# Kernel tuning notes

Hardware: AMD Instinct MI355X
Metric: run time of the kernel (lower is better)

## Reference

```python
import jax, jax.numpy as jnp
import numpy as np

B, S, D, H = 2, 2048, 2048, 16
HD = D // H  # head_dim = 128
ROPE_BASE = 10000.0


def _rope_tables(seq_len, head_dim, base, dtype):
    inv_freq = 1.0 / (base ** (jnp.arange(0, head_dim, 2, dtype=jnp.float32) / head_dim))
    t = jnp.arange(seq_len, dtype=jnp.float32)
    freqs = jnp.einsum('s,d->sd', t, inv_freq)           # [S, HD/2]
    emb = jnp.concatenate([freqs, freqs], axis=-1)        # [S, HD]
    return jnp.cos(emb).astype(dtype), jnp.sin(emb).astype(dtype)


def _rotate_half(x):
    half = x.shape[-1] // 2
    return jnp.concatenate([-x[..., half:], x[..., :half]], axis=-1)


def setup_inputs() -> dict:
    key = jax.random.key(0)
    kx, kq, kk, kv, ko = jax.random.split(key, 5)
    std = 0.02
    return {
        'x': jax.random.normal(kx, (B, S, D), dtype=jnp.float32),
        'Wq': jax.random.normal(kq, (D, D), dtype=jnp.float32) * std,
        'Wk': jax.random.normal(kk, (D, D), dtype=jnp.float32) * std,
        'Wv': jax.random.normal(kv, (D, D), dtype=jnp.float32) * std,
        'Wo': jax.random.normal(ko, (D, D), dtype=jnp.float32) * std,
    }


def reference(x, Wq, Wk, Wv, Wo):
    b, s, d = x.shape
    scale = HD ** -0.5
    # projections (nn.Linear: x @ W.T), split heads -> [b, h, s, hd]
    q = (x @ Wq.T).reshape(b, s, H, HD).transpose(0, 2, 1, 3)
    k = (x @ Wk.T).reshape(b, s, H, HD).transpose(0, 2, 1, 3)
    v = (x @ Wv.T).reshape(b, s, H, HD).transpose(0, 2, 1, 3)
    cos, sin = _rope_tables(s, HD, ROPE_BASE, x.dtype)    # [s, hd]
    q = q * cos + _rotate_half(q) * sin
    k = k * cos + _rotate_half(k) * sin
    scores = jnp.einsum('bhqd,bhkd->bhqk', q, k) * scale  # [b,h,s,s]
    causal = jnp.triu(jnp.ones((s, s), dtype=bool), k=1)
    scores = jnp.where(causal, jnp.float32(-jnp.inf).astype(scores.dtype), scores)
    attn = jax.nn.softmax(scores, axis=-1)
    out = jnp.einsum('bhqk,bhkd->bhqd', attn, v)
    out = out.transpose(0, 2, 1, 3).reshape(b, s, d)
    return out @ Wo.T
```

## Files before the change

### kernel.cpp

```cpp
#include <hip/hip_runtime.h>
#include <hip/hip_bf16.h>
#include <cstdint>
#include <cstddef>

#define B_ 2
#define S_ 2048
#define D_ 2048
#define H_ 16
#define HD_ 128

typedef __bf16 bf16_t;
typedef __bf16 bf16x8 __attribute__((ext_vector_type(8)));
typedef __bf16 bf16x4 __attribute__((ext_vector_type(4)));
typedef short s16x4 __attribute__((ext_vector_type(4)));
typedef float f32x4 __attribute__((ext_vector_type(4)));

__device__ __forceinline__ void async16(const bf16_t* g, bf16_t* l) {
    __builtin_amdgcn_global_load_lds(
        (const __attribute__((address_space(1))) unsigned int*)g,
        (__attribute__((address_space(3))) unsigned int*)l, 16, 0, 0);
}

__device__ __forceinline__ f32x4 mfma16x16x16_bf16(bf16x4 a, bf16x4 b, f32x4 c) {
#if __has_builtin(__builtin_amdgcn_mfma_f32_16x16x16_bf16)
    return __builtin_amdgcn_mfma_f32_16x16x16_bf16(a, b, c, 0, 0, 0);
#elif __has_builtin(__builtin_amdgcn_mfma_f32_16x16x16bf16_1k)
    return __builtin_amdgcn_mfma_f32_16x16x16bf16_1k(
        __builtin_bit_cast(s16x4, a), __builtin_bit_cast(s16x4, b), c, 0, 0, 0);
#else
    f32x4 d = c;
    asm("v_mfma_f32_16x16x16_bf16 %0, %1, %2, %0" : "+v"(d) : "v"(a), "v"(b));
    return d;
#endif
}

__global__ void f2b_multi(const float* __restrict__ x, const float* __restrict__ wq,
                          const float* __restrict__ wk, const float* __restrict__ wv,
                          const float* __restrict__ wo, bf16_t* __restrict__ xb,
                          bf16_t* __restrict__ wqb, bf16_t* __restrict__ wkb,
                          bf16_t* __restrict__ wvb, bf16_t* __restrict__ wob) {
    const float* in; bf16_t* out;
    float sc = 1.0f;
    switch (blockIdx.y) {
        case 0: in = x;            out = xb;            break;
        case 1: in = x + 4194304;  out = xb + 4194304;  break;
        case 2: in = wq;           out = wqb; sc = 0.08838834764831845f; break;
        case 3: in = wk;           out = wkb;           break;
        case 4: in = wv;           out = wvb;           break;
        default: in = wo;          out = wob;           break;
    }
    int i = (blockIdx.x * blockDim.x + threadIdx.x) * 4;
    float4 v = *(const float4*)(in + i);
    bf16x4 o = { (bf16_t)(v.x * sc), (bf16_t)(v.y * sc), (bf16_t)(v.z * sc), (bf16_t)(v.w * sc) };
    *(bf16x4*)(out + i) = o;
}

__global__ void rope_kernel(bf16_t* __restrict__ q, bf16_t* __restrict__ k) {
    int idx = blockIdx.x * blockDim.x + threadIdx.x;
    bf16_t* p = (blockIdx.y == 0) ? q : k;
    int i0 = (idx & 7) * 8;
    int rest = idx >> 3;
    int h = rest & (H_ - 1);
    int row = rest >> 4;
    int s = row & (S_ - 1);
    size_t base = (size_t)row * D_ + (size_t)h * HD_ + i0;
    bf16x8 x0 = *(bf16x8*)(p + base);
    bf16x8 x1 = *(bf16x8*)(p + base + 64);
    bf16x8 o0, o1;
#pragma unroll
    for (int j = 0; j < 8; ++j) {
        float inv = __expf(-(float)(i0 + j) * 0.14391156831212787f);
        float ang = (float)s * inv;
        float sn, c;
        __sincosf(ang, &sn, &c);
        float a = (float)x0[j], bb = (float)x1[j];
        o0[j] = (bf16_t)(a * c - bb * sn);
        o1[j] = (bf16_t)(bb * c + a * sn);
    }
    *(bf16x8*)(p + base) = o0;
    *(bf16x8*)(p + base + 64) = o1;
}


__global__ __launch_bounds__(512, 2) void gemm_qkv(const bf16_t* __restrict__ A,
                                                   const bf16_t* __restrict__ Wq,
                                                   const bf16_t* __restrict__ Wk,
                                                   const bf16_t* __restrict__ Wv,
                                                   bf16_t* __restrict__ qb,
                                                   bf16_t* __restrict__ kb,
                                                   bf16_t* __restrict__ vtb) {
    __shared__ __align__(16) bf16_t lds[49152];
    const int K = D_;
    const int NT = K / 64;
    int t = threadIdx.x;
    int w = t >> 6, lane = t & 63, lo = lane & 15, hi = lane >> 4;
    int seg = blockIdx.x >> 4;
    int n0 = (blockIdx.x & 15) * 128;
    int m0 = blockIdx.y * 256;
    const bf16_t* Bt = (seg == 0) ? Wq : (seg == 1) ? Wk : Wv;
    int wm = w >> 2, wn = w & 3;
    f32x4 acc[8][2] = {};
    int srowA = w * 32 + (lane >> 3);
    int srowB = w * 16 + (lane >> 3);
    int scol = ((lane & 7) ^ (lane >> 3)) * 8;
    const bf16_t* gA = A  + (size_t)(m0 + srowA) * K + scol;
    const bf16_t* gB = Bt + (size_t)(n0 + srowB) * K + scol;

    auto STAGE = [&](int c, int kt) {
        bf16_t* dA = lds + c * 24576 + w * 2048 + lane * 8;
        bf16_t* dB = lds + c * 24576 + 16384 + w * 1024 + lane * 8;
        int k0 = kt * 64;
#pragma unroll
        for (int i = 0; i < 4; ++i)
            async16(gA + (size_t)(i * 8) * K + k0, dA + i * 512);
#pragma unroll
        for (int i = 0; i < 2; ++i)
            async16(gB + (size_t)(i * 8) * K + k0, dB + i * 512);
    };

    STAGE(0, 0);
    STAGE(1, 1);
    asm volatile("s_waitcnt vmcnt(6)" ::: "memory");
    __builtin_amdgcn_sched_barrier(0);
    __builtin_amdgcn_s_barrier();

#pragma unroll 1
    for (int tt = 0; tt < NT; ++tt) {
        int cur = tt & 1;
        const bf16_t* As = lds + cur * 24576;
        const bf16_t* Bs = As + 16384;
#pragma unroll
        for (int p = 0; p < 2; ++p) {
            bf16x8 af[4][2], bfv[2][2];
#pragma unroll
            for (int ms = 0; ms < 4; ++ms) {
                int row = wm * 128 + p * 64 + ms * 16 + lo;
#pragma unroll
                for (int kk = 0; kk < 2; ++kk)
                    af[ms][kk] = *(const bf16x8*)(As + row * 64 + (((kk * 4 + hi) ^ (lo & 7)) * 8));
            }
#pragma unroll
            for (int ns = 0; ns < 2; ++ns) {
                int row = wn * 32 + ns * 16 + lo;
#pragma unroll
                for (int kk = 0; kk < 2; ++kk)
                    bfv[ns][kk] = *(const bf16x8*)(Bs + row * 64 + (((kk * 4 + hi) ^ (lo & 7)) * 8));
            }
            __builtin_amdgcn_sched_barrier(0);
            __builtin_amdgcn_s_barrier();
            asm volatile("s_waitcnt lgkmcnt(0)" ::: "memory");
            __builtin_amdgcn_sched_barrier(0);
            __builtin_amdgcn_s_setprio(1);
#pragma unroll
            for (int ms = 0; ms < 4; ++ms)
#pragma unroll
                for (int ns = 0; ns < 2; ++ns)
#pragma unroll
                    for (int kk = 0; kk < 2; ++kk)
                        acc[p * 4 + ms][ns] = __builtin_amdgcn_mfma_f32_16x16x32_bf16(
                            af[ms][kk], bfv[ns][kk], acc[p * 4 + ms][ns], 0, 0, 0);
            __builtin_amdgcn_s_setprio(0);
            __builtin_amdgcn_sched_barrier(0);
            __builtin_amdgcn_s_barrier();
        }
        if (tt + 2 < NT) {
            STAGE(cur, tt + 2);
            asm volatile("s_waitcnt vmcnt(6)" ::: "memory");
            __builtin_amdgcn_sched_barrier(0);
            __builtin_amdgcn_s_barrier();
        } else if (tt + 1 < NT) {
            asm volatile("s_waitcnt vmcnt(0)" ::: "memory");
            __builtin_amdgcn_sched_barrier(0);
            __builtin_amdgcn_s_barrier();
        }
    }

    if (seg < 2) {
        bf16_t* C = (seg == 0) ? qb : kb;
#pragma unroll
        for (int ms = 0; ms < 8; ++ms)
#pragma unroll
            for (int ns = 0; ns < 2; ++ns)
#pragma unroll
                for (int r = 0; r < 4; ++r)
                    C[(size_t)(m0 + wm * 128 + ms * 16 + hi * 4 + r) * D_ + n0 + wn * 32 + ns * 16 + lo] =
                        (bf16_t)acc[ms][ns][r];
    } else {
#pragma unroll
        for (int ms = 0; ms < 8; ++ms) {
            int mrow = m0 + wm * 128 + ms * 16 + hi * 4;
            int bb = mrow >> 11, s = mrow & (S_ - 1);
#pragma unroll
            for (int ns = 0; ns < 2; ++ns) {
                int d = n0 + wn * 32 + ns * 16 + lo;
                bf16x4 pv = { (bf16_t)acc[ms][ns][0], (bf16_t)acc[ms][ns][1],
                              (bf16_t)acc[ms][ns][2], (bf16_t)acc[ms][ns][3] };
                *(bf16x4*)(vtb + (size_t)bb * D_ * S_ + (size_t)d * S_ + s) = pv;
            }
        }
    }
}

__global__ __launch_bounds__(512, 2) void gemm_bt_f32(const bf16_t* __restrict__ A,
                                                      const bf16_t* __restrict__ Bt,
                                                      float* __restrict__ C,
                                                      int M, int N, int K) {
    (void)M;
    __shared__ __align__(16) bf16_t lds[49152];
    const int NT = K / 64;
    int t = threadIdx.x;
    int w = t >> 6, lane = t & 63, lo = lane & 15, hi = lane >> 4;
    int n0 = blockIdx.x * 128;
    int m0 = blockIdx.y * 256;
    int wm = w >> 2, wn = w & 3;
    f32x4 acc[8][2] = {};
    int srowA = w * 32 + (lane >> 3);
    int srowB = w * 16 + (lane >> 3);
    int scol = ((lane & 7) ^ (lane >> 3)) * 8;
    const bf16_t* gA = A  + (size_t)(m0 + srowA) * K + scol;
    const bf16_t* gB = Bt + (size_t)(n0 + srowB) * K + scol;

    auto STAGE = [&](int c, int kt) {
        bf16_t* dA = lds + c * 24576 + w * 2048 + lane * 8;
        bf16_t* dB = lds + c * 24576 + 16384 + w * 1024 + lane * 8;
        int k0 = kt * 64;
#pragma unroll
        for (int i = 0; i < 4; ++i)
            async16(gA + (size_t)(i * 8) * K + k0, dA + i * 512);
#pragma unroll
        for (int i = 0; i < 2; ++i)
            async16(gB + (size_t)(i * 8) * K + k0, dB + i * 512);
    };

    STAGE(0, 0);
    STAGE(1, 1);
    asm volatile("s_waitcnt vmcnt(6)" ::: "memory");
    __builtin_amdgcn_sched_barrier(0);
    __builtin_amdgcn_s_barrier();

#pragma unroll 1
    for (int tt = 0; tt < NT; ++tt) {
        int cur = tt & 1;
        const bf16_t* As = lds + cur * 24576;
        const bf16_t* Bs = As + 16384;
#pragma unroll
        for (int p = 0; p < 2; ++p) {
            bf16x8 af[4][2], bfv[2][2];
#pragma unroll
            for (int ms = 0; ms < 4; ++ms) {
                int row = wm * 128 + p * 64 + ms * 16 + lo;
#pragma unroll
                for (int kk = 0; kk < 2; ++kk)
                    af[ms][kk] = *(const bf16x8*)(As + row * 64 + (((kk * 4 + hi) ^ (lo & 7)) * 8));
            }
#pragma unroll
            for (int ns = 0; ns < 2; ++ns) {
                int row = wn * 32 + ns * 16 + lo;
#pragma unroll
                for (int kk = 0; kk < 2; ++kk)
                    bfv[ns][kk] = *(const bf16x8*)(Bs + row * 64 + (((kk * 4 + hi) ^ (lo & 7)) * 8));
            }
            __builtin_amdgcn_sched_barrier(0);
            __builtin_amdgcn_s_barrier();
            asm volatile("s_waitcnt lgkmcnt(0)" ::: "memory");
            __builtin_amdgcn_sched_barrier(0);
            __builtin_amdgcn_s_setprio(1);
#pragma unroll
            for (int ms = 0; ms < 4; ++ms)
#pragma unroll
                for (int ns = 0; ns < 2; ++ns)
#pragma unroll
                    for (int kk = 0; kk < 2; ++kk)
                        acc[p * 4 + ms][ns] = __builtin_amdgcn_mfma_f32_16x16x32_bf16(
                            af[ms][kk], bfv[ns][kk], acc[p * 4 + ms][ns], 0, 0, 0);
            __builtin_amdgcn_s_setprio(0);
            __builtin_amdgcn_sched_barrier(0);
            __builtin_amdgcn_s_barrier();
        }
        if (tt + 2 < NT) {
            STAGE(cur, tt + 2);
            asm volatile("s_waitcnt vmcnt(6)" ::: "memory");
            __builtin_amdgcn_sched_barrier(0);
            __builtin_amdgcn_s_barrier();
        } else if (tt + 1 < NT) {
            asm volatile("s_waitcnt vmcnt(0)" ::: "memory");
            __builtin_amdgcn_sched_barrier(0);
            __builtin_amdgcn_s_barrier();
        }
    }

#pragma unroll
    for (int ms = 0; ms < 8; ++ms)
#pragma unroll
        for (int ns = 0; ns < 2; ++ns)
#pragma unroll
            for (int r = 0; r < 4; ++r)
                C[(size_t)(m0 + wm * 128 + ms * 16 + hi * 4 + r) * N + n0 + wn * 32 + ns * 16 + lo] =
                    acc[ms][ns][r];
}

__global__ __launch_bounds__(256) void attn_kernel(const bf16_t* __restrict__ q,
                                                   const bf16_t* __restrict__ k,
                                                   const bf16_t* __restrict__ vt,
                                                   bf16_t* __restrict__ o) {
    __shared__ __align__(16) bf16_t Ks[128 * 128];
    __shared__ __align__(16) bf16_t Vs[128 * 128];
    int t = threadIdx.x;
    int w = t >> 6, lane = t & 63, lo = lane & 15, hi = lane >> 4;
    int bx = blockIdx.x;
    int b = blockIdx.y >> 4, h = blockIdx.y & 15;
    const size_t head_off = (size_t)b * S_ * D_ + (size_t)h * HD_;
    const size_t vhead_off = ((size_t)b * D_ + (size_t)h * HD_) * S_;

#pragma unroll 1
    for (int pass = 0; pass < 2; ++pass) {
        int qt = pass ? (31 - bx) : bx;
        int q0 = qt * 64;
        int qg = q0 + w * 16 + lo;
        bf16x8 aq[4];
#pragma unroll
        for (int c = 0; c < 4; ++c)
            aq[c] = *(const bf16x8*)(q + head_off + (size_t)qg * D_ + c * 32 + hi * 8);

        float l_part = 0.f;
        f32x4 oacc[8] = {};
        int nkt = (qt >> 1) + 1;
        for (int kt = 0; kt < nkt; ++kt) {
            int k0 = kt * 128;
            __syncthreads();
#pragma unroll
            for (int i = 0; i < 8; ++i) {
                int chunk = w * 8 + i;
                int r = chunk * 4 + (lane >> 4);
                int lc = (lane & 15) ^ (r & 15);
                async16(k + head_off + (size_t)(k0 + r) * D_ + lc * 8,
                        Ks + chunk * 512 + lane * 8);
            }
#pragma unroll
            for (int i = 0; i < 8; ++i) {
                int chunk = w * 8 + i;
                int d = chunk * 4 + (lane >> 4);
                int lc = (lane & 15) ^ (d & 15);
                async16(vt + vhead_off + (size_t)d * S_ + k0 + lc * 8,
                        Vs + chunk * 512 + lane * 8);
            }
            __syncthreads();

            if (k0 <= q0 + w * 16 + 15) {
                f32x4 sacc[8] = {};
#pragma unroll
                for (int c = 0; c < 4; ++c) {
#pragma unroll
                    for (int nt = 0; nt < 8; ++nt) {
                        int row = nt * 16 + lo;
                        int pc = (c * 4 + hi) ^ lo;
                        bf16x8 ak = *(const bf16x8*)(Ks + row * 128 + pc * 8);
                        sacc[nt] = __builtin_amdgcn_mfma_f32_16x16x32_bf16(ak, aq[c], sacc[nt], 0, 0, 0);
                    }
                }
                bool diag = (k0 + 127 > q0 + w * 16);
                bf16x4 pf[8];
#pragma unroll
                for (int nt = 0; nt < 8; ++nt) {
#pragma unroll
                    for (int r = 0; r < 4; ++r) {
                        float e = __expf(fminf(sacc[nt][r], 60.f));
                        if (diag) {
                            int kg = k0 + nt * 16 + hi * 4 + r;
                            if (kg > qg) e = 0.f;
                        }
                        l_part += e;
                        pf[nt][r] = (bf16_t)e;
                    }
                }
#pragma unroll
                for (int nt = 0; nt < 8; ++nt) {
                    int kkb = nt * 16 + hi * 4;
                    int c16 = kkb >> 3, rem = kkb & 7;
#pragma unroll
                    for (int dt = 0; dt < 8; ++dt) {
                        int d = dt * 16 + lo;
                        bf16x4 av = *(const bf16x4*)(Vs + d * 128 + (c16 ^ (d & 15)) * 8 + rem);
                        oacc[dt] = mfma16x16x16_bf16(av, pf[nt], oacc[dt]);
                    }
                }
            }
        }
        float l = l_part;
        l += __shfl_xor(l, 16);
        l += __shfl_xor(l, 32);
        float rl = 1.0f / l;
#pragma unroll
        for (int dt = 0; dt < 8; ++dt) {
            bf16x4 ov = { (bf16_t)(oacc[dt][0] * rl), (bf16_t)(oacc[dt][1] * rl),
                          (bf16_t)(oacc[dt][2] * rl), (bf16_t)(oacc[dt][3] * rl) };
            *(bf16x4*)(o + head_off + (size_t)qg * D_ + dt * 16 + hi * 4) = ov;
        }
    }
}

extern "C" void kernel_launch(void* const* d_in, const int* in_sizes, int n_in,
                              void* d_out, int out_size, void* d_ws, size_t ws_size,
                              hipStream_t stream) {
    (void)in_sizes; (void)n_in; (void)out_size; (void)ws_size;
    const float* x  = (const float*)d_in[0];
    const float* Wq = (const float*)d_in[1];
    const float* Wk = (const float*)d_in[2];
    const float* Wv = (const float*)d_in[3];
    const float* Wo = (const float*)d_in[4];
    char* ws = (char*)d_ws;
    bf16_t* xb  = (bf16_t*)(ws);
    bf16_t* Wqb = (bf16_t*)(ws + 16777216);
    bf16_t* Wkb = (bf16_t*)(ws + 25165824);
    bf16_t* Wvb = (bf16_t*)(ws + 33554432);
    bf16_t* Wob = (bf16_t*)(ws + 41943040);
    bf16_t* qb  = (bf16_t*)(ws + 50331648);
    bf16_t* kb  = (bf16_t*)(ws + 67108864);
    bf16_t* vtb = (bf16_t*)(ws + 83886080);
    bf16_t* ob  = (bf16_t*)(ws + 100663296);
    float* out = (float*)d_out;

    f2b_multi<<<dim3(4096, 6), 256, 0, stream>>>(x, Wq, Wk, Wv, Wo, xb, Wqb, Wkb, Wvb, Wob);

    gemm_qkv<<<dim3(48, 16), 512, 0, stream>>>(xb, Wqb, Wkb, Wvb, qb, kb, vtb);

    rope_kernel<<<dim3((B_ * S_ * H_ * 8) / 256, 2), 256, 0, stream>>>(qb, kb);

    attn_kernel<<<dim3(16, B_ * H_), 256, 0, stream>>>(qb, kb, vtb, ob);

    gemm_bt_f32<<<dim3(D_ / 128, (B_ * S_) / 256), 512, 0, stream>>>(ob, Wob, out, B_ * S_, D_, D_);
}
```

Baseline: 408.1 us.

## Triple-buffer QKV GEMM with interleaved prefetch; simplify output projection GEMM

```diff
diff --git a/kernel.cpp b/kernel.cpp
--- a/kernel.cpp
+++ b/kernel.cpp
@@ -81,7 +81,6 @@
     *(bf16x8*)(p + base + 64) = o1;
 }
 
-
 __global__ __launch_bounds__(512, 2) void gemm_qkv(const bf16_t* __restrict__ A,
                                                    const bf16_t* __restrict__ Wq,
                                                    const bf16_t* __restrict__ Wk,
@@ -89,7 +88,7 @@
                                                    bf16_t* __restrict__ qb,
                                                    bf16_t* __restrict__ kb,
                                                    bf16_t* __restrict__ vtb) {
-    __shared__ __align__(16) bf16_t lds[49152];
+    __shared__ __align__(16) bf16_t lds[73728];
     const int K = D_;
     const int NT = K / 64;
     int t = threadIdx.x;
@@ -105,36 +104,37 @@
     int scol = ((lane & 7) ^ (lane >> 3)) * 8;
     const bf16_t* gA = A  + (size_t)(m0 + srowA) * K + scol;
     const bf16_t* gB = Bt + (size_t)(n0 + srowB) * K + scol;
-
-    auto STAGE = [&](int c, int kt) {
-        bf16_t* dA = lds + c * 24576 + w * 2048 + lane * 8;
-        bf16_t* dB = lds + c * 24576 + 16384 + w * 1024 + lane * 8;
-        int k0 = kt * 64;
-#pragma unroll
-        for (int i = 0; i < 4; ++i)
-            async16(gA + (size_t)(i * 8) * K + k0, dA + i * 512);
-#pragma unroll
-        for (int i = 0; i < 2; ++i)
-            async16(gB + (size_t)(i * 8) * K + k0, dB + i * 512);
-    };
-
-    STAGE(0, 0);
-    STAGE(1, 1);
+    bf16_t* const wAd = lds + w * 2048 + lane * 8;
+    bf16_t* const wBd = lds + 16384 + w * 1024 + lane * 8;
+
+#pragma unroll
+    for (int i = 0; i < 4; ++i) async16(gA + (size_t)(i * 8) * K, wAd + i * 512);
+#pragma unroll
+    for (int i = 0; i < 2; ++i) async16(gB + (size_t)(i * 8) * K, wBd + i * 512);
+#pragma unroll
+    for (int i = 0; i < 4; ++i) async16(gA + (size_t)(i * 8) * K + 64, wAd + 24576 + i * 512);
+#pragma unroll
+    for (int i = 0; i < 2; ++i) async16(gB + (size_t)(i * 8) * K + 64, wBd + 24576 + i * 512);
     asm volatile("s_waitcnt vmcnt(6)" ::: "memory");
     __builtin_amdgcn_sched_barrier(0);
     __builtin_amdgcn_s_barrier();
 
+    int cur = 0;
 #pragma unroll 1
     for (int tt = 0; tt < NT; ++tt) {
-        int cur = tt & 1;
         const bf16_t* As = lds + cur * 24576;
         const bf16_t* Bs = As + 16384;
-#pragma unroll
-        for (int p = 0; p < 2; ++p) {
+        int nb = cur + 2; if (nb >= 3) nb -= 3;
+        bf16_t* dA = wAd + nb * 24576;
+        bf16_t* dB = wBd + nb * 24576;
+        int k2 = (tt + 2) * 64;
+        bool st = (tt + 2 < NT);
+
+        {
             bf16x8 af[4][2], bfv[2][2];
 #pragma unroll
             for (int ms = 0; ms < 4; ++ms) {
-                int row = wm * 128 + p * 64 + ms * 16 + lo;
+                int row = wm * 128 + ms * 16 + lo;
 #pragma unroll
                 for (int kk = 0; kk < 2; ++kk)
                     af[ms][kk] = *(const bf16x8*)(As + row * 64 + (((kk * 4 + hi) ^ (lo & 7)) * 8));
@@ -146,6 +146,11 @@
                 for (int kk = 0; kk < 2; ++kk)
                     bfv[ns][kk] = *(const bf16x8*)(Bs + row * 64 + (((kk * 4 + hi) ^ (lo & 7)) * 8));
             }
+            if (st) {
+                async16(gA + k2, dA);
+                async16(gA + (size_t)8 * K + k2, dA + 512);
+                async16(gB + k2, dB);
+            }
             __builtin_amdgcn_sched_barrier(0);
             __builtin_amdgcn_s_barrier();
             asm volatile("s_waitcnt lgkmcnt(0)" ::: "memory");
@@ -157,22 +162,56 @@
                 for (int ns = 0; ns < 2; ++ns)
 #pragma unroll
                     for (int kk = 0; kk < 2; ++kk)
-                        acc[p * 4 + ms][ns] = __builtin_amdgcn_mfma_f32_16x16x32_bf16(
-                            af[ms][kk], bfv[ns][kk], acc[p * 4 + ms][ns], 0, 0, 0);
+                        acc[ms][ns] = __builtin_amdgcn_mfma_f32_16x16x32_bf16(
+                            af[ms][kk], bfv[ns][kk], acc[ms][ns], 0, 0, 0);
             __builtin_amdgcn_s_setprio(0);
             __builtin_amdgcn_sched_barrier(0);
             __builtin_amdgcn_s_barrier();
         }
-        if (tt + 2 < NT) {
-            STAGE(cur, tt + 2);
-            asm volatile("s_waitcnt vmcnt(6)" ::: "memory");
+        {
+            bf16x8 af[4][2], bfv[2][2];
+#pragma unroll
+            for (int ms = 0; ms < 4; ++ms) {
+                int row = wm * 128 + 64 + ms * 16 + lo;
+#pragma unroll
+                for (int kk = 0; kk < 2; ++kk)
+                    af[ms][kk] = *(const bf16x8*)(As + row * 64 + (((kk * 4 + hi) ^ (lo & 7)) * 8));
+            }
+#pragma unroll
+            for (int ns = 0; ns < 2; ++ns) {
+                int row = wn * 32 + ns * 16 + lo;
+#pragma unroll
+                for (int kk = 0; kk < 2; ++kk)
+                    bfv[ns][kk] = *(const bf16x8*)(Bs + row * 64 + (((kk * 4 + hi) ^ (lo & 7)) * 8));
+            }
+            if (st) {
+                async16(gA + (size_t)16 * K + k2, dA + 1024);
+                async16(gA + (size_t)24 * K + k2, dA + 1536);
+                async16(gB + (size_t)8 * K + k2, dB + 512);
+            }
             __builtin_amdgcn_sched_barrier(0);
             __builtin_amdgcn_s_barrier();
-        } else if (tt + 1 < NT) {
-            asm volatile("s_waitcnt vmcnt(0)" ::: "memory");
+            asm volatile("s_waitcnt lgkmcnt(0)" ::: "memory");
+            __builtin_amdgcn_sched_barrier(0);
+            __builtin_amdgcn_s_setprio(1);
+#pragma unroll
+            for (int ms = 0; ms < 4; ++ms)
+#pragma unroll
+                for (int ns = 0; ns < 2; ++ns)
+#pragma unroll
+                    for (int kk = 0; kk < 2; ++kk)
+                        acc[4 + ms][ns] = __builtin_amdgcn_mfma_f32_16x16x32_bf16(
+                            af[ms][kk], bfv[ns][kk], acc[4 + ms][ns], 0, 0, 0);
+            __builtin_amdgcn_s_setprio(0);
+            __builtin_amdgcn_sched_barrier(0);
+            if (st)
+                asm volatile("s_waitcnt vmcnt(6)" ::: "memory");
+            else if (tt + 1 < NT)
+                asm volatile("s_waitcnt vmcnt(0)" ::: "memory");
             __builtin_amdgcn_sched_barrier(0);
             __builtin_amdgcn_s_barrier();
         }
+        cur = cur + 1; if (cur == 3) cur = 0;
     }
 
     if (seg < 2) {
@@ -201,102 +240,55 @@
     }
 }
 
-__global__ __launch_bounds__(512, 2) void gemm_bt_f32(const bf16_t* __restrict__ A,
-                                                      const bf16_t* __restrict__ Bt,
-                                                      float* __restrict__ C,
-                                                      int M, int N, int K) {
-    (void)M;
-    __shared__ __align__(16) bf16_t lds[49152];
-    const int NT = K / 64;
+__global__ __launch_bounds__(256) void gemm_bt_f32(const bf16_t* __restrict__ A,
+                                                   const bf16_t* __restrict__ Bt,
+                                                   float* __restrict__ C,
+                                                   int M, int N, int K) {
+    __shared__ __align__(16) bf16_t As[128 * 64];
+    __shared__ __align__(16) bf16_t Bs[128 * 64];
     int t = threadIdx.x;
     int w = t >> 6, lane = t & 63, lo = lane & 15, hi = lane >> 4;
-    int n0 = blockIdx.x * 128;
-    int m0 = blockIdx.y * 256;
-    int wm = w >> 2, wn = w & 3;
-    f32x4 acc[8][2] = {};
-    int srowA = w * 32 + (lane >> 3);
-    int srowB = w * 16 + (lane >> 3);
+    int m0 = blockIdx.y * 128, n0 = blockIdx.x * 128;
+    int wm = (w & 1) * 64, wn = (w >> 1) * 64;
+    f32x4 acc[4][4] = {};
+    int srow = w * 32 + (lane >> 3);
     int scol = ((lane & 7) ^ (lane >> 3)) * 8;
-    const bf16_t* gA = A  + (size_t)(m0 + srowA) * K + scol;
-    const bf16_t* gB = Bt + (size_t)(n0 + srowB) * K + scol;
-
-    auto STAGE = [&](int c, int kt) {
-        bf16_t* dA = lds + c * 24576 + w * 2048 + lane * 8;
-        bf16_t* dB = lds + c * 24576 + 16384 + w * 1024 + lane * 8;
-        int k0 = kt * 64;
-#pragma unroll
-        for (int i = 0; i < 4; ++i)
-            async16(gA + (size_t)(i * 8) * K + k0, dA + i * 512);
-#pragma unroll
-        for (int i = 0; i < 2; ++i)
-            async16(gB + (size_t)(i * 8) * K + k0, dB + i * 512);
-    };
-
-    STAGE(0, 0);
-    STAGE(1, 1);
-    asm volatile("s_waitcnt vmcnt(6)" ::: "memory");
-    __builtin_amdgcn_sched_barrier(0);
-    __builtin_amdgcn_s_barrier();
-
-#pragma unroll 1
-    for (int tt = 0; tt < NT; ++tt) {
-        int cur = tt & 1;
-        const bf16_t* As = lds + cur * 24576;
-        const bf16_t* Bs = As + 16384;
-#pragma unroll
-        for (int p = 0; p < 2; ++p) {
-            bf16x8 af[4][2], bfv[2][2];
-#pragma unroll
-            for (int ms = 0; ms < 4; ++ms) {
-                int row = wm * 128 + p * 64 + ms * 16 + lo;
-#pragma unroll
-                for (int kk = 0; kk < 2; ++kk)
-                    af[ms][kk] = *(const bf16x8*)(As + row * 64 + (((kk * 4 + hi) ^ (lo & 7)) * 8));
-            }
-#pragma unroll
-            for (int ns = 0; ns < 2; ++ns) {
-                int row = wn * 32 + ns * 16 + lo;
-#pragma unroll
-                for (int kk = 0; kk < 2; ++kk)
-                    bfv[ns][kk] = *(const bf16x8*)(Bs + row * 64 + (((kk * 4 + hi) ^ (lo & 7)) * 8));
-            }
-            __builtin_amdgcn_sched_barrier(0);
-            __builtin_amdgcn_s_barrier();
-            asm volatile("s_waitcnt lgkmcnt(0)" ::: "memory");
-            __builtin_amdgcn_sched_barrier(0);
-            __builtin_amdgcn_s_setprio(1);
+    const bf16_t* gA = A  + (size_t)(m0 + srow) * K + scol;
+    const bf16_t* gB = Bt + (size_t)(n0 + srow) * K + scol;
+    bf16_t* lA = As + w * 2048 + lane * 8;
+    bf16_t* lB = Bs + w * 2048 + lane * 8;
+    for (int k0 = 0; k0 < K; k0 += 64) {
+#pragma unroll
+        for (int i = 0; i < 4; ++i) {
+            async16(gA + (size_t)(i * 8) * K + k0, lA + i * 512);
+            async16(gB + (size_t)(i * 8) * K + k0, lB + i * 512);
+        }
+        __syncthreads();
+#pragma unroll
+        for (int kk = 0; kk < 2; ++kk) {
+            bf16x8 af[4], bfr[4];
+            int pc = (kk * 4 + hi) ^ (lo & 7);
 #pragma unroll
             for (int ms = 0; ms < 4; ++ms)
-#pragma unroll
-                for (int ns = 0; ns < 2; ++ns)
-#pragma unroll
-                    for (int kk = 0; kk < 2; ++kk)
-                        acc[p * 4 + ms][ns] = __builtin_amdgcn_mfma_f32_16x16x32_bf16(
-                            af[ms][kk], bfv[ns][kk], acc[p * 4 + ms][ns], 0, 0, 0);
-            __builtin_amdgcn_s_setprio(0);
-            __builtin_amdgcn_sched_barrier(0);
-            __builtin_amdgcn_s_barrier();
-        }
-        if (tt + 2 < NT) {
-            STAGE(cur, tt + 2);
-            asm volatile("s_waitcnt vmcnt(6)" ::: "memory");
-            __builtin_amdgcn_sched_barrier(0);
-            __builtin_amdgcn_s_barrier();
-        } else if (tt + 1 < NT) {
-            asm volatile("s_waitcnt vmcnt(0)" ::: "memory");
-            __builtin_amdgcn_sched_barrier(0);
-            __builtin_amdgcn_s_barrier();
-        }
-    }
-
-#pragma unroll
-    for (int ms = 0; ms < 8; ++ms)
-#pragma unroll
-        for (int ns = 0; ns < 2; ++ns)
+                af[ms] = *(const bf16x8*)(As + (wm + ms * 16 + lo) * 64 + pc * 8);
+#pragma unroll
+            for (int ns = 0; ns < 4; ++ns)
+                bfr[ns] = *(const bf16x8*)(Bs + (wn + ns * 16 + lo) * 64 + pc * 8);
+#pragma unroll
+            for (int ms = 0; ms < 4; ++ms)
+#pragma unroll
+                for (int ns = 0; ns < 4; ++ns)
+                    acc[ms][ns] = __builtin_amdgcn_mfma_f32_16x16x32_bf16(af[ms], bfr[ns], acc[ms][ns], 0, 0, 0);
+        }
+        __syncthreads();
+    }
+#pragma unroll
+    for (int ms = 0; ms < 4; ++ms)
+#pragma unroll
+        for (int ns = 0; ns < 4; ++ns)
 #pragma unroll
             for (int r = 0; r < 4; ++r)
-                C[(size_t)(m0 + wm * 128 + ms * 16 + hi * 4 + r) * N + n0 + wn * 32 + ns * 16 + lo] =
-                    acc[ms][ns][r];
+                C[(size_t)(m0 + wm + ms * 16 + hi * 4 + r) * N + n0 + wn + ns * 16 + lo] = acc[ms][ns][r];
 }
 
 __global__ __launch_bounds__(256) void attn_kernel(const bf16_t* __restrict__ q,
@@ -428,5 +420,5 @@
 
     attn_kernel<<<dim3(16, B_ * H_), 256, 0, stream>>>(qb, kb, vtb, ob);
 
-    gemm_bt_f32<<<dim3(D_ / 128, (B_ * S_) / 256), 512, 0, stream>>>(ob, Wob, out, B_ * S_, D_, D_);
-}
+    gemm_bt_f32<<<dim3(D_ / 128, (B_ * S_) / 128), 256, 0, stream>>>(ob, Wob, out, B_ * S_, D_, D_);
+}
```

Result: faster. 393.6 us (-3.6%).
